# Optimization experiments

Hardware: AMD Instinct MI355X
Metric: run time of the kernel (lower is better)

Reference implementation:

```python
import jax, jax.numpy as jnp
import numpy as np

TEMPERATURE = 0.5
EPS = 1e-8  # matches F.cosine_similarity eps clamp


def setup_inputs() -> dict:
    key = jax.random.key(0)
    k1, k2 = jax.random.split(key)
    logits = jax.random.normal(k1, (8192, 256), dtype=jnp.float32)
    label = jax.random.randint(k2, (8192,), 0, 10, dtype=jnp.int64)
    return {"logits": logits, "label": label}


def reference(logits, label):
    n = label.shape[0]
    # pairwise cosine similarity via normalize + GEMM (same math as the
    # broadcasted F.cosine_similarity, without the O(n^2 d) intermediate)
    norms = jnp.maximum(jnp.linalg.norm(logits, axis=1, keepdims=True), EPS)
    xn = logits / norms                       # [n, d]
    sim_matrix = xn @ xn.T                    # [n, n]

    eye = jnp.eye(n, dtype=sim_matrix.dtype)
    mask = (label[:, None] == label[None, :]).astype(sim_matrix.dtype)  # same-label (incl. diag)

    e = jnp.exp(sim_matrix / TEMPERATURE) * (1.0 - eye)  # zero diagonal
    sim = mask * e                            # same-label positives
    no_sim_sum = jnp.sum(e - sim, axis=1)     # [n] row sums of different-label terms
    sim_sum = sim + no_sim_sum[:, None]       # denominator per entry
    ratio = sim / sim_sum

    # zeros (different-label entries) get +1 via (1 - mask), diagonal gets +1 via eye -> -log(1) = 0
    loss_mat = -jnp.log((1.0 - mask) + ratio + eye)
    return jnp.sum(loss_mat) / (2 * n)
```

## Files before the change

kernel.cpp:

```cpp
#include <hip/hip_runtime.h>
#include <cstdint>
#include <cstddef>

typedef float  f32x4  __attribute__((ext_vector_type(4)));
typedef long long i64;
typedef unsigned char uchar;

#define N_ROWS 8192
#define KDIM   256
#define TEMP_INV 2.0f
#define LOG2E  1.4426950408889634f
#define EXPC   (TEMP_INV * LOG2E)

#define AS1 __attribute__((address_space(1)))
#define AS3 __attribute__((address_space(3)))

__global__ __launch_bounds__(256) void prep(const float* __restrict__ logits,
        const int* __restrict__ label, uchar* __restrict__ xn8,
        int* __restrict__ perm, int* __restrict__ labelPerm,
        int* __restrict__ classStart, int* __restrict__ cumTiles)
{
    __shared__ int lcnt[256][10];
    __shared__ int cstart[11];
    __shared__ int ccount[10];
    const int tid = threadIdx.x;
    const int bid = blockIdx.x;

    if (bid < 2048) {
        const int p = bid * 4 + (tid >> 6);
        const int lane = tid & 63;
        float4 v = reinterpret_cast<const float4*>(logits + (size_t)p * KDIM)[lane];
        float ss = v.x*v.x + v.y*v.y + v.z*v.z + v.w*v.w;
        #pragma unroll
        for (int off = 32; off >= 1; off >>= 1) ss += __shfl_xor(ss, off, 64);
        float inv = 1.0f / fmaxf(sqrtf(ss), 1e-8f);
        int pk = __builtin_amdgcn_cvt_pk_fp8_f32(v.x * inv, v.y * inv, 0, false);
        pk     = __builtin_amdgcn_cvt_pk_fp8_f32(v.z * inv, v.w * inv, pk, true);
        reinterpret_cast<unsigned int*>(xn8 + (size_t)p * KDIM)[lane] = (unsigned int)pk;
        return;
    }

    const int wave = tid >> 6, lane = tid & 63;
    const int beg = tid * 32, end = beg + 32;
    int loc[10] = {0,0,0,0,0,0,0,0,0,0};
    for (int i = beg; i < end; ++i) {
        int c = label[i]; c = (c < 0) ? 0 : (c > 9 ? 9 : c);
        loc[c]++;
    }
    #pragma unroll
    for (int c = 0; c < 10; ++c) lcnt[tid][c] = loc[c];
    __syncthreads();

    for (int c = wave; c < 10; c += 4) {
        int s0 = lcnt[lane*4+0][c], s1 = lcnt[lane*4+1][c];
        int s2 = lcnt[lane*4+2][c], s3 = lcnt[lane*4+3][c];
        int tot = s0 + s1 + s2 + s3;
        int incl = tot;
        #pragma unroll
        for (int d = 1; d < 64; d <<= 1) {
            int up = __shfl_up(incl, d, 64);
            if (lane >= d) incl += up;
        }
        int excl = incl - tot;
        lcnt[lane*4+0][c] = excl;
        lcnt[lane*4+1][c] = excl + s0;
        lcnt[lane*4+2][c] = excl + s0 + s1;
        lcnt[lane*4+3][c] = excl + s0 + s1 + s2;
        if (lane == 63) ccount[c] = incl;
    }
    __syncthreads();

    if (tid == 0) {
        int run = 0, runT = 0;
        for (int c = 0; c < 10; ++c) {
            cstart[c] = run; classStart[c] = run;
            int tpc = (ccount[c] + 127) >> 7;
            cumTiles[c] = runT;
            run  += ccount[c];
            runT += tpc * (tpc + 1) / 2;
        }
        cstart[10] = run; classStart[10] = run; cumTiles[10] = runT;
    }
    __syncthreads();

    int ofs[10];
    #pragma unroll
    for (int c = 0; c < 10; ++c) ofs[c] = lcnt[tid][c];
    for (int i = beg; i < end; ++i) {
        int c = label[i]; c = (c < 0) ? 0 : (c > 9 ? 9 : c);
        int pos = cstart[c] + ofs[c]++;
        perm[pos] = i;
        labelPerm[pos] = c;
    }
}

__device__ __forceinline__ void stage2(const uchar* sA0, const uchar* sA1,
        const uchar* sB0, const uchar* sB1, int kb,
        uchar* As, uchar* Bs, int lo0, int lo1)
{
    __builtin_amdgcn_global_load_lds((const AS1 void*)(sA0 + kb), (AS3 void*)(As + lo0), 16, 0, 0);
    __builtin_amdgcn_global_load_lds((const AS1 void*)(sA1 + kb), (AS3 void*)(As + lo1), 16, 0, 0);
    __builtin_amdgcn_global_load_lds((const AS1 void*)(sB0 + kb), (AS3 void*)(Bs + lo0), 16, 0, 0);
    __builtin_amdgcn_global_load_lds((const AS1 void*)(sB1 + kb), (AS3 void*)(Bs + lo1), 16, 0, 0);
}

__device__ __forceinline__ void read_frags8(const uchar* As, const uchar* Bs,
        i64 (&a)[2][4], i64 (&b)[2][4], int wave, int lane)
{
    const int wr = wave >> 1, wc = wave & 1;
    const int lrow = lane & 15, kgrp = lane >> 4;
    const int ch = kgrp >> 1, half = kgrp & 1;
    #pragma unroll
    for (int kk = 0; kk < 2; ++kk) {
        const int c16 = kk * 2 + ch;
        #pragma unroll
        for (int mi = 0; mi < 4; ++mi) {
            const int row = wr*64 + mi*16 + lrow;
            a[kk][mi] = *reinterpret_cast<const i64*>(As + (size_t)row * 64 + ((c16 ^ (row & 3)) * 16) + half * 8);
        }
        #pragma unroll
        for (int ni = 0; ni < 4; ++ni) {
            const int row = wc*64 + ni*16 + lrow;
            b[kk][ni] = *reinterpret_cast<const i64*>(Bs + (size_t)row * 64 + ((c16 ^ (row & 3)) * 16) + half * 8);
        }
    }
}

__device__ __forceinline__ void mfma_frags8(i64 (&a)[2][4], i64 (&b)[2][4], f32x4 (&acc)[4][4])
{
    #pragma unroll
    for (int kk = 0; kk < 2; ++kk)
        #pragma unroll
        for (int mi = 0; mi < 4; ++mi)
            #pragma unroll
            for (int ni = 0; ni < 4; ++ni)
                acc[mi][ni] = __builtin_amdgcn_mfma_f32_16x16x32_fp8_fp8(a[kk][mi], b[kk][ni], acc[mi][ni], 0, 0, 0);
}

#define PIPE8_READS_RELEASE(Ac, Bc)                                  \
    i64 a[2][4], b[2][4];                                            \
    read_frags8(Ac, Bc, a, b, wave, lane);                           \
    __builtin_amdgcn_sched_barrier(0);                               \
    asm volatile("s_waitcnt lgkmcnt(0)" ::: "memory");               \
    __builtin_amdgcn_sched_barrier(0);                               \
    __builtin_amdgcn_s_barrier();                                    \
    __builtin_amdgcn_sched_barrier(0);

#define PIPE8_MFMA()                                                 \
    __builtin_amdgcn_s_setprio(1);                                   \
    mfma_frags8(a, b, acc);                                          \
    __builtin_amdgcn_s_setprio(0);

#define PIPE8_TAIL(N)                                                \
    __builtin_amdgcn_sched_barrier(0);                               \
    asm volatile("s_waitcnt vmcnt(" #N ")" ::: "memory");            \
    __builtin_amdgcn_s_barrier();                                    \
    __builtin_amdgcn_sched_barrier(0);

#define KLOOP_FP8()                                                           \
    stage2(sA0, sA1, sB0, sB1, 0,   As0, Bs0, lo0, lo1);                      \
    stage2(sA0, sA1, sB0, sB1, 64,  As1, Bs1, lo0, lo1);                      \
    asm volatile("s_waitcnt vmcnt(4)" ::: "memory");                          \
    __builtin_amdgcn_s_barrier();                                             \
    __builtin_amdgcn_sched_barrier(0);                                        \
    {                                                                         \
        PIPE8_READS_RELEASE(As0, Bs0)                                         \
        stage2(sA0, sA1, sB0, sB1, 128, As0, Bs0, lo0, lo1);                  \
        PIPE8_MFMA()                                                          \
        PIPE8_TAIL(4)                                                         \
    }                                                                         \
    {                                                                         \
        PIPE8_READS_RELEASE(As1, Bs1)                                         \
        stage2(sA0, sA1, sB0, sB1, 192, As1, Bs1, lo0, lo1);                  \
        PIPE8_MFMA()                                                          \
        PIPE8_TAIL(4)                                                         \
    }                                                                         \
    {                                                                         \
        PIPE8_READS_RELEASE(As0, Bs0)                                         \
        PIPE8_MFMA()                                                          \
        PIPE8_TAIL(0)                                                         \
    }                                                                         \
    {                                                                         \
        PIPE8_READS_RELEASE(As1, Bs1)                                         \
        PIPE8_MFMA()                                                          \
    }

#define TILE_SRC_SETUP(rowBase, colBase)                                      \
    const int ci0 = wave * 64 + lane, ci1 = 256 + wave * 64 + lane;           \
    const int r0 = ci0 >> 2, r1 = ci1 >> 2;                                   \
    const int c0 = (ci0 & 3) ^ (r0 & 3), c1 = (ci1 & 3) ^ (r1 & 3);           \
    const uchar* sA0 = xn8 + (size_t)perm[(rowBase) + r0] * KDIM + c0 * 16;   \
    const uchar* sA1 = xn8 + (size_t)perm[(rowBase) + r1] * KDIM + c1 * 16;   \
    const uchar* sB0 = xn8 + (size_t)perm[(colBase) + r0] * KDIM + c0 * 16;   \
    const uchar* sB1 = xn8 + (size_t)perm[(colBase) + r1] * KDIM + c1 * 16;   \
    const int lo0 = ci0 * 16, lo1 = ci1 * 16;

__global__ __launch_bounds__(256, 4) void phase1_gemm(const uchar* __restrict__ xn8,
        const int* __restrict__ perm, const int* __restrict__ labelPerm,
        float* __restrict__ pD)
{
    __shared__ __align__(16) char pool[32768];
    uchar* As0 = (uchar*)(pool);
    uchar* Bs0 = (uchar*)(pool + 8192);
    uchar* As1 = (uchar*)(pool + 16384);
    uchar* Bs1 = (uchar*)(pool + 24576);
    float* rowD = (float*)pool;
    float* colD = (float*)(pool + 16384);
    __shared__ int labLDS[256];

    const int tid = threadIdx.x;
    const int wave = tid >> 6, lane = tid & 63;

    int t = blockIdx.x, bi = 0;
    while (t >= 64 - bi) { t -= 64 - bi; ++bi; }
    const int bj = bi + t;
    const bool isDiag = (bi == bj);
    const int rowBase = bi * 128, colBase = bj * 128;

    if (labelPerm[rowBase] == labelPerm[colBase + 127]) {
        if (tid < 128)       pD[(size_t)bj * N_ROWS + rowBase + tid] = 0.f;
        else if (!isDiag)    pD[(size_t)bi * N_ROWS + colBase + tid - 128] = 0.f;
        return;
    }

    labLDS[tid] = labelPerm[(tid < 128) ? (rowBase + tid) : (colBase + tid - 128)];
    TILE_SRC_SETUP(rowBase, colBase)
    __builtin_amdgcn_sched_barrier(0);

    f32x4 acc[4][4] = {};
    KLOOP_FP8()

    const int wr = wave >> 1, wc = wave & 1;
    const int lrow = lane & 15, lgrp = lane >> 4;
    float colAcc[4] = {0.f, 0.f, 0.f, 0.f};
    #pragma unroll
    for (int mi = 0; mi < 4; ++mi) {
        #pragma unroll
        for (int reg = 0; reg < 4; ++reg) {
            const int tr = wr * 64 + mi * 16 + lgrp * 4 + reg;
            const int rl = labLDS[tr];
            float rowAcc = 0.f;
            #pragma unroll
            for (int ni = 0; ni < 4; ++ni) {
                const int tc = wc * 64 + ni * 16 + lrow;
                float e = __builtin_amdgcn_exp2f(acc[mi][ni][reg] * EXPC);
                float ed = (rl != labLDS[128 + tc]) ? e : 0.f;
                rowAcc += ed;
                colAcc[ni] += ed;
            }
            rowD[tr * 32 + wc * 16 + lrow] = rowAcc;
        }
    }
    if (!isDiag) {
        #pragma unroll
        for (int ni = 0; ni < 4; ++ni) {
            const int tc = wc * 64 + ni * 16 + lrow;
            colD[tc * 8 + wr * 4 + lgrp] = colAcc[ni];
        }
    }
    __syncthreads();

    if (tid < 128) {
        const float* p = rowD + tid * 32;
        float s = 0.f;
        #pragma unroll
        for (int k = 0; k < 8; ++k) {
            f32x4 v = *reinterpret_cast<const f32x4*>(p + k * 4);
            s += v[0] + v[1] + v[2] + v[3];
        }
        pD[(size_t)bj * N_ROWS + rowBase + tid] = s;
    } else if (!isDiag) {
        const int c2 = tid - 128;
        const float* p = colD + c2 * 8;
        f32x4 v0 = *reinterpret_cast<const f32x4*>(p);
        f32x4 v1 = *reinterpret_cast<const f32x4*>(p + 4);
        pD[(size_t)bi * N_ROWS + colBase + c2] =
            v0[0] + v0[1] + v0[2] + v0[3] + v1[0] + v1[1] + v1[2] + v1[3];
    }
}

__global__ __launch_bounds__(256, 4) void phase3_loss(const uchar* __restrict__ xn8,
        const int* __restrict__ perm, const float* __restrict__ pD,
        const int* __restrict__ classStart, const int* __restrict__ cumTiles,
        float* __restrict__ partial)
{
    __shared__ __align__(16) char pool[32768];
    uchar* As0 = (uchar*)(pool);
    uchar* Bs0 = (uchar*)(pool + 8192);
    uchar* As1 = (uchar*)(pool + 16384);
    uchar* Bs1 = (uchar*)(pool + 24576);
    __shared__ float redF[256];
    __shared__ float DarrH[256];
    __shared__ float DarrR[128];
    __shared__ float DarrC[128];
    __shared__ int   meta[22];

    const int tid = threadIdx.x;
    const int wave = tid >> 6, lane = tid & 63;

    if (tid < 11) { meta[tid] = classStart[tid]; meta[11 + tid] = cumTiles[tid]; }
    __syncthreads();
    const int nTiles = meta[11 + 10];

    float tileSum = 0.f;
    for (int b = blockIdx.x; b < nTiles; b += 512) {
        __syncthreads();

        int c = 0;
        while (c < 9 && b >= meta[11 + c + 1]) ++c;
        const int s = meta[c], e = meta[c + 1];
        const int nc = e - s;
        const int tps = (nc + 127) >> 7;
        int lt = b - meta[11 + c];
        int ti = 0;
        while (lt >= tps - ti) { lt -= tps - ti; ++ti; }
        const int tj = ti + lt;
        const bool isDiagT = (ti == tj);
        const int rowBase = s + ti * 128, colBase = s + tj * 128;

        {
            int r = rowBase + (tid & 127); if (r > N_ROWS - 1) r = N_ROWS - 1;
            const int half = tid >> 7;
            float d = 0.f;
            #pragma unroll 4
            for (int sl = half * 32; sl < half * 32 + 32; ++sl)
                d += pD[(size_t)sl * N_ROWS + r];
            DarrH[(tid & 127) * 2 + half] = d;
        }
        __syncthreads();
        if (tid < 128) DarrR[tid] = DarrH[tid * 2] + DarrH[tid * 2 + 1];
        __syncthreads();
        if (!isDiagT) {
            int r = colBase + (tid & 127); if (r > N_ROWS - 1) r = N_ROWS - 1;
            const int half = tid >> 7;
            float d = 0.f;
            #pragma unroll 4
            for (int sl = half * 32; sl < half * 32 + 32; ++sl)
                d += pD[(size_t)sl * N_ROWS + r];
            DarrH[(tid & 127) * 2 + half] = d;
            __syncthreads();
            if (tid < 128) DarrC[tid] = DarrH[tid * 2] + DarrH[tid * 2 + 1];
        }

        TILE_SRC_SETUP(rowBase, colBase)
        asm volatile("s_waitcnt vmcnt(0)" ::: "memory");
        __syncthreads();

        f32x4 acc[4][4] = {};
        KLOOP_FP8()

        const int wr = wave >> 1, wc = wave & 1;
        const int lrow = lane & 15, lgrp = lane >> 4;
        #pragma unroll
        for (int mi = 0; mi < 4; ++mi) {
            #pragma unroll
            for (int reg = 0; reg < 4; ++reg) {
                const int tr = wr * 64 + mi * 16 + lgrp * 4 + reg;
                const int r = rowBase + tr;
                if (r < e) {
                    const float Dr = DarrR[tr];
                    #pragma unroll
                    for (int ni = 0; ni < 4; ++ni) {
                        const int tc = wc * 64 + ni * 16 + lrow;
                        const int cg = colBase + tc;
                        if (cg < e) {
                            float sim = acc[mi][ni][reg];
                            float ev = __builtin_amdgcn_exp2f(sim * EXPC);
                            if (isDiagT) {
                                if (cg != r)
                                    tileSum += __logf(ev + Dr) - TEMP_INV * sim;
                            } else {
                                tileSum += __logf(ev + Dr) + __logf(ev + DarrC[tc])
                                         - 2.0f * TEMP_INV * sim;
                            }
                        }
                    }
                }
            }
        }
    }

    __syncthreads();
    redF[tid] = tileSum;
    __syncthreads();
    for (int st = 128; st > 0; st >>= 1) {
        if (tid < st) redF[tid] += redF[tid + st];
        __syncthreads();
    }
    if (tid == 0) partial[blockIdx.x] = redF[0];
}

__global__ void phase4_final(const float* __restrict__ partial, float* __restrict__ out)
{
    __shared__ float red[256];
    const int tid = threadIdx.x;
    float s = partial[tid] + partial[tid + 256];
    red[tid] = s;
    __syncthreads();
    for (int st = 128; st > 0; st >>= 1) {
        if (tid < st) red[tid] += red[tid + st];
        __syncthreads();
    }
    if (tid == 0) out[0] = red[0] * (1.0f / 16384.0f);
}

extern "C" void kernel_launch(void* const* d_in, const int* in_sizes, int n_in,
                              void* d_out, int out_size, void* d_ws, size_t ws_size,
                              hipStream_t stream)
{
    const float* logits = (const float*)d_in[0];
    const int*   label  = (const int*)d_in[1];
    float* out = (float*)d_out;

    char* ws = (char*)d_ws;
    uchar*  xn8       = (uchar*)(ws);
    float*  pD        = (float*)(ws + (2u << 20));
    int*    perm      = (int*)(ws + (4u << 20));
    int*    labelPerm = (int*)(ws + (4u << 20) + (32u << 10));
    int*    classStart= (int*)(ws + (4u << 20) + (64u << 10));
    int*    cumTiles  = (int*)(ws + (4u << 20) + (64u << 10) + 256);
    float*  partial   = (float*)(ws + (4u << 20) + (128u << 10));

    hipLaunchKernelGGL(prep, dim3(2049), dim3(256), 0, stream,
                       logits, label, xn8, perm, labelPerm, classStart, cumTiles);
    hipLaunchKernelGGL(phase1_gemm, dim3(2080), dim3(256), 0, stream,
                       xn8, perm, labelPerm, pD);
    hipLaunchKernelGGL(phase3_loss, dim3(512), dim3(256), 0, stream,
                       xn8, perm, pD, classStart, cumTiles, partial);
    hipLaunchKernelGGL(phase4_final, dim3(1), dim3(256), 0, stream,
                       partial, out);
}
```

Before: 72.37 us.

## Replace double-buffered K pipeline with one-shot full-K LDS staging

Drops the two-buffer, four-step K-loop and its many barriers. Both GEMM kernels now load the whole 128x256 fp8 A and B tiles into LDS (64KB) in one go, then run all MFMAs after a single barrier. In the loss kernel the tile loads are issued before the pD row-sum reads so the two sets of memory traffic overlap. The cost is twice the LDS per block, with launch bounds lowered to 2 blocks per CU, so there is less latency hiding across blocks.

```diff
diff --git a/kernel.cpp b/kernel.cpp
--- a/kernel.cpp
+++ b/kernel.cpp
@@ -94,116 +94,60 @@
     }
 }
 
-__device__ __forceinline__ void stage2(const uchar* sA0, const uchar* sA1,
-        const uchar* sB0, const uchar* sB1, int kb,
-        uchar* As, uchar* Bs, int lo0, int lo1)
-{
-    __builtin_amdgcn_global_load_lds((const AS1 void*)(sA0 + kb), (AS3 void*)(As + lo0), 16, 0, 0);
-    __builtin_amdgcn_global_load_lds((const AS1 void*)(sA1 + kb), (AS3 void*)(As + lo1), 16, 0, 0);
-    __builtin_amdgcn_global_load_lds((const AS1 void*)(sB0 + kb), (AS3 void*)(Bs + lo0), 16, 0, 0);
-    __builtin_amdgcn_global_load_lds((const AS1 void*)(sB1 + kb), (AS3 void*)(Bs + lo1), 16, 0, 0);
-}
-
-__device__ __forceinline__ void read_frags8(const uchar* As, const uchar* Bs,
-        i64 (&a)[2][4], i64 (&b)[2][4], int wave, int lane)
+__device__ __forceinline__ void stage_oneshot(const uchar* __restrict__ xn8,
+        const int* __restrict__ perm, int rowBase, int colBase,
+        uchar* As, uchar* Bs, int tid)
+{
+    const int t4 = tid >> 4;
+    const int ch = (tid & 15) ^ t4;
+    #pragma unroll
+    for (int i = 0; i < 8; ++i) {
+        const int row = i * 16 + t4;
+        int rA = rowBase + row; if (rA > N_ROWS - 1) rA = N_ROWS - 1;
+        int rB = colBase + row; if (rB > N_ROWS - 1) rB = N_ROWS - 1;
+        const int lds_off = (i * 256 + tid) * 16;
+        const uchar* gA = xn8 + (size_t)perm[rA] * KDIM + ch * 16;
+        const uchar* gB = xn8 + (size_t)perm[rB] * KDIM + ch * 16;
+        __builtin_amdgcn_global_load_lds((const AS1 void*)gA, (AS3 void*)(As + lds_off), 16, 0, 0);
+        __builtin_amdgcn_global_load_lds((const AS1 void*)gB, (AS3 void*)(Bs + lds_off), 16, 0, 0);
+    }
+}
+
+__device__ __forceinline__ void mfma_oneshot(const uchar* As, const uchar* Bs,
+        f32x4 (&acc)[4][4], int wave, int lane)
 {
     const int wr = wave >> 1, wc = wave & 1;
     const int lrow = lane & 15, kgrp = lane >> 4;
-    const int ch = kgrp >> 1, half = kgrp & 1;
-    #pragma unroll
-    for (int kk = 0; kk < 2; ++kk) {
-        const int c16 = kk * 2 + ch;
+    const int ch2 = kgrp >> 1, half8 = (kgrp & 1) * 8;
+    #pragma unroll
+    for (int s = 0; s < 8; ++s) {
+        const int c16 = s * 2 + ch2;
+        i64 a[4], b[4];
         #pragma unroll
         for (int mi = 0; mi < 4; ++mi) {
             const int row = wr*64 + mi*16 + lrow;
-            a[kk][mi] = *reinterpret_cast<const i64*>(As + (size_t)row * 64 + ((c16 ^ (row & 3)) * 16) + half * 8);
+            a[mi] = *reinterpret_cast<const i64*>(As + (size_t)row * 256 + ((c16 ^ lrow) * 16) + half8);
         }
         #pragma unroll
         for (int ni = 0; ni < 4; ++ni) {
             const int row = wc*64 + ni*16 + lrow;
-            b[kk][ni] = *reinterpret_cast<const i64*>(Bs + (size_t)row * 64 + ((c16 ^ (row & 3)) * 16) + half * 8);
-        }
-    }
-}
-
-__device__ __forceinline__ void mfma_frags8(i64 (&a)[2][4], i64 (&b)[2][4], f32x4 (&acc)[4][4])
-{
-    #pragma unroll
-    for (int kk = 0; kk < 2; ++kk)
+            b[ni] = *reinterpret_cast<const i64*>(Bs + (size_t)row * 256 + ((c16 ^ lrow) * 16) + half8);
+        }
         #pragma unroll
         for (int mi = 0; mi < 4; ++mi)
             #pragma unroll
             for (int ni = 0; ni < 4; ++ni)
-                acc[mi][ni] = __builtin_amdgcn_mfma_f32_16x16x32_fp8_fp8(a[kk][mi], b[kk][ni], acc[mi][ni], 0, 0, 0);
-}
-
-#define PIPE8_READS_RELEASE(Ac, Bc)                                  \
-    i64 a[2][4], b[2][4];                                            \
-    read_frags8(Ac, Bc, a, b, wave, lane);                           \
-    __builtin_amdgcn_sched_barrier(0);                               \
-    asm volatile("s_waitcnt lgkmcnt(0)" ::: "memory");               \
-    __builtin_amdgcn_sched_barrier(0);                               \
-    __builtin_amdgcn_s_barrier();                                    \
-    __builtin_amdgcn_sched_barrier(0);
-
-#define PIPE8_MFMA()                                                 \
-    __builtin_amdgcn_s_setprio(1);                                   \
-    mfma_frags8(a, b, acc);                                          \
-    __builtin_amdgcn_s_setprio(0);
-
-#define PIPE8_TAIL(N)                                                \
-    __builtin_amdgcn_sched_barrier(0);                               \
-    asm volatile("s_waitcnt vmcnt(" #N ")" ::: "memory");            \
-    __builtin_amdgcn_s_barrier();                                    \
-    __builtin_amdgcn_sched_barrier(0);
-
-#define KLOOP_FP8()                                                           \
-    stage2(sA0, sA1, sB0, sB1, 0,   As0, Bs0, lo0, lo1);                      \
-    stage2(sA0, sA1, sB0, sB1, 64,  As1, Bs1, lo0, lo1);                      \
-    asm volatile("s_waitcnt vmcnt(4)" ::: "memory");                          \
-    __builtin_amdgcn_s_barrier();                                             \
-    __builtin_amdgcn_sched_barrier(0);                                        \
-    {                                                                         \
-        PIPE8_READS_RELEASE(As0, Bs0)                                         \
-        stage2(sA0, sA1, sB0, sB1, 128, As0, Bs0, lo0, lo1);                  \
-        PIPE8_MFMA()                                                          \
-        PIPE8_TAIL(4)                                                         \
-    }                                                                         \
-    {                                                                         \
-        PIPE8_READS_RELEASE(As1, Bs1)                                         \
-        stage2(sA0, sA1, sB0, sB1, 192, As1, Bs1, lo0, lo1);                  \
-        PIPE8_MFMA()                                                          \
-        PIPE8_TAIL(4)                                                         \
-    }                                                                         \
-    {                                                                         \
-        PIPE8_READS_RELEASE(As0, Bs0)                                         \
-        PIPE8_MFMA()                                                          \
-        PIPE8_TAIL(0)                                                         \
-    }                                                                         \
-    {                                                                         \
-        PIPE8_READS_RELEASE(As1, Bs1)                                         \
-        PIPE8_MFMA()                                                          \
-    }
-
-#define TILE_SRC_SETUP(rowBase, colBase)                                      \
-    const int ci0 = wave * 64 + lane, ci1 = 256 + wave * 64 + lane;           \
-    const int r0 = ci0 >> 2, r1 = ci1 >> 2;                                   \
-    const int c0 = (ci0 & 3) ^ (r0 & 3), c1 = (ci1 & 3) ^ (r1 & 3);           \
-    const uchar* sA0 = xn8 + (size_t)perm[(rowBase) + r0] * KDIM + c0 * 16;   \
-    const uchar* sA1 = xn8 + (size_t)perm[(rowBase) + r1] * KDIM + c1 * 16;   \
-    const uchar* sB0 = xn8 + (size_t)perm[(colBase) + r0] * KDIM + c0 * 16;   \
-    const uchar* sB1 = xn8 + (size_t)perm[(colBase) + r1] * KDIM + c1 * 16;   \
-    const int lo0 = ci0 * 16, lo1 = ci1 * 16;
-
-__global__ __launch_bounds__(256, 4) void phase1_gemm(const uchar* __restrict__ xn8,
+                acc[mi][ni] = __builtin_amdgcn_mfma_f32_16x16x32_fp8_fp8(a[mi], b[ni], acc[mi][ni], 0, 0, 0);
+    }
+}
+
+__global__ __launch_bounds__(256, 2) void phase1_gemm(const uchar* __restrict__ xn8,
         const int* __restrict__ perm, const int* __restrict__ labelPerm,
         float* __restrict__ pD)
 {
-    __shared__ __align__(16) char pool[32768];
-    uchar* As0 = (uchar*)(pool);
-    uchar* Bs0 = (uchar*)(pool + 8192);
-    uchar* As1 = (uchar*)(pool + 16384);
-    uchar* Bs1 = (uchar*)(pool + 24576);
+    __shared__ __align__(16) char pool[65536];
+    uchar* As = (uchar*)(pool);
+    uchar* Bs = (uchar*)(pool + 32768);
     float* rowD = (float*)pool;
     float* colD = (float*)(pool + 16384);
     __shared__ int labLDS[256];
@@ -223,12 +167,13 @@
         return;
     }
 
+    stage_oneshot(xn8, perm, rowBase, colBase, As, Bs, tid);
     labLDS[tid] = labelPerm[(tid < 128) ? (rowBase + tid) : (colBase + tid - 128)];
-    TILE_SRC_SETUP(rowBase, colBase)
-    __builtin_amdgcn_sched_barrier(0);
+    __syncthreads();
 
     f32x4 acc[4][4] = {};
-    KLOOP_FP8()
+    mfma_oneshot(As, Bs, acc, wave, lane);
+    __syncthreads();
 
     const int wr = wave >> 1, wc = wave & 1;
     const int lrow = lane & 15, lgrp = lane >> 4;
@@ -279,16 +224,14 @@
     }
 }
 
-__global__ __launch_bounds__(256, 4) void phase3_loss(const uchar* __restrict__ xn8,
+__global__ __launch_bounds__(256, 2) void phase3_loss(const uchar* __restrict__ xn8,
         const int* __restrict__ perm, const float* __restrict__ pD,
         const int* __restrict__ classStart, const int* __restrict__ cumTiles,
         float* __restrict__ partial)
 {
-    __shared__ __align__(16) char pool[32768];
-    uchar* As0 = (uchar*)(pool);
-    uchar* Bs0 = (uchar*)(pool + 8192);
-    uchar* As1 = (uchar*)(pool + 16384);
-    uchar* Bs1 = (uchar*)(pool + 24576);
+    __shared__ __align__(16) char pool[65536];
+    uchar* As = (uchar*)(pool);
+    uchar* Bs = (uchar*)(pool + 32768);
     __shared__ float redF[256];
     __shared__ float DarrH[256];
     __shared__ float DarrR[128];
@@ -318,6 +261,8 @@
         const bool isDiagT = (ti == tj);
         const int rowBase = s + ti * 128, colBase = s + tj * 128;
 
+        stage_oneshot(xn8, perm, rowBase, colBase, As, Bs, tid);
+
         {
             int r = rowBase + (tid & 127); if (r > N_ROWS - 1) r = N_ROWS - 1;
             const int half = tid >> 7;
@@ -341,13 +286,10 @@
             __syncthreads();
             if (tid < 128) DarrC[tid] = DarrH[tid * 2] + DarrH[tid * 2 + 1];
         }
-
-        TILE_SRC_SETUP(rowBase, colBase)
-        asm volatile("s_waitcnt vmcnt(0)" ::: "memory");
         __syncthreads();
 
         f32x4 acc[4][4] = {};
-        KLOOP_FP8()
+        mfma_oneshot(As, Bs, acc, wave, lane);
 
         const int wr = wave >> 1, wc = wave & 1;
         const int lrow = lane & 15, lgrp = lane >> 4;
```

After: 67.97 us, median of 2. 6.1% less time.
